# Performance work log

Hardware: AMD Instinct MI355X
Metric: run time of the kernel (lower is better)

The kernel has to match this reference:

```python
import jax, jax.numpy as jnp
import numpy as np
import math
from math import factorial

MUL = 128            # channel multiplicity of in1 and out
LS = [0, 1, 2]       # l values of the three irreps in each input/output
N_PATH_W = MUL * 1 * MUL  # uvw weight block per path (mul2 == 1)

# ---- Wigner 3j (real basis), following e3nn's construction ----

def _su2_cg(j1, m1, j2, m2, j3, m3):
    if m3 != m1 + m2:
        return 0.0
    vmin = int(max(-j1 + j2 + m3, -j1 + m1, 0))
    vmax = int(min(j2 + j3 + m1, j3 - j1 + j2, j3 + m3))
    if vmax < vmin:
        return 0.0
    f = lambda n: factorial(int(round(n)))
    pref = (2 * j3 + 1) * (f(j3 + j1 - j2) * f(j3 - j1 + j2) * f(j1 + j2 - j3) * f(j3 + m3) * f(j3 - m3)) / (
        f(j1 + j2 + j3 + 1) * f(j1 - m1) * f(j1 + m1) * f(j2 - m2) * f(j2 + m2))
    S = 0.0
    for v in range(vmin, vmax + 1):
        S += (-1) ** (v + j2 + m2) * (f(j2 + j3 + m1 - v) * f(j1 - m1 + v)) / (
            f(v) * f(j3 - j1 + j2 - v) * f(j3 + m3 - v) * f(v + j1 - j2 - m3))
    return math.sqrt(pref) * S


def _q(l):
    # change of basis real -> complex spherical harmonics (e3nn convention)
    q = np.zeros((2 * l + 1, 2 * l + 1), dtype=np.complex128)
    for m in range(-l, 0):
        q[l + m, l + abs(m)] = 1 / math.sqrt(2)
        q[l + m, l - abs(m)] = -1j / math.sqrt(2)
    q[l, l] = 1
    for m in range(1, l + 1):
        q[l + m, l + abs(m)] = (-1) ** m / math.sqrt(2)
        q[l + m, l - abs(m)] = 1j * (-1) ** m / math.sqrt(2)
    return (-1j) ** l * q


def _w3j(l1, l2, l3):
    C = np.zeros((2 * l1 + 1, 2 * l2 + 1, 2 * l3 + 1))
    for m1 in range(-l1, l1 + 1):
        for m2 in range(-l2, l2 + 1):
            m3 = m1 + m2
            if abs(m3) <= l3:
                C[m1 + l1, m2 + l2, m3 + l3] = _su2_cg(l1, m1, l2, m2, l3, m3)
    Q1, Q2, Q3 = _q(l1), _q(l2), _q(l3)
    Cc = np.einsum('ij,kl,mn,ikn->jlm', Q1, Q2, np.conj(Q3.T), C.astype(np.complex128))
    Cr, Ci = Cc.real, Cc.imag
    Cp = Cr if np.linalg.norm(Cr) >= np.linalg.norm(Ci) else Ci
    return (Cp / np.linalg.norm(Cp)).astype(np.float32)

# allowed (l1, l2) -> l_out paths for 0e/1o/2e x 0e/1o/2e -> 0e/1o/2e
PATHS = [(0, 0, 0), (0, 1, 1), (0, 2, 2), (1, 0, 1), (1, 1, 0), (1, 1, 2),
         (1, 2, 1), (2, 0, 2), (2, 1, 1), (2, 2, 0), (2, 2, 2)]
# path_normalization='element': alpha = (2*l_out+1) / sum over paths to same out of mul1*mul2
_FAN = {o: sum(MUL for (_, _, c) in PATHS if c == o) for o in LS}
PW = {o: math.sqrt((2 * o + 1) / _FAN[o]) for o in LS}
W3J = {(a, b, c): _w3j(a, b, c) for (a, b, c) in PATHS}


def _split1(x):
    # [N, 1152] -> list of [N, 128, 2l+1]
    parts, off = [], 0
    for l in LS:
        d = MUL * (2 * l + 1)
        parts.append(x[:, off:off + d].reshape(-1, MUL, 2 * l + 1))
        off += d
    return parts


def _split2(x):
    # [N, 9] -> list of [N, 2l+1]
    parts, off = [], 0
    for l in LS:
        parts.append(x[:, off:off + 2 * l + 1])
        off += 2 * l + 1
    return parts


def _fctp(x1, x2, weight):
    xs1, xs2 = _split1(x1), _split2(x2)
    N = x1.shape[0]
    outs = [jnp.zeros((N, MUL, 2 * l + 1), x1.dtype) for l in LS]
    off = 0
    for (l1, l2, lo) in PATHS:
        w = weight[off:off + N_PATH_W].reshape(MUL, MUL)  # [u, w] (v == 1)
        off += N_PATH_W
        C = jnp.asarray(W3J[(l1, l2, lo)])  # [2l1+1, 2l2+1, 2lo+1]
        t = jnp.einsum('ijk,nui,nj->nuk', C, xs1[l1], xs2[l2])
        outs[lo] = outs[lo] + PW[lo] * jnp.einsum('uw,nuk->nwk', w, t)
    return jnp.concatenate([o.reshape(N, -1) for o in outs], axis=1)


def setup_inputs() -> dict:
    key = jax.random.key(0)
    k1, k2, k3 = jax.random.split(key, 3)
    N = 20000
    return {
        'x1': jax.random.normal(k1, (N, MUL * 9), dtype=jnp.float32),
        'x2': jax.random.normal(k2, (N, 9), dtype=jnp.float32),
        'weight': jax.random.normal(k3, (len(PATHS) * N_PATH_W,), dtype=jnp.float32),
    }


def reference(x1, x2, weight):
    return _fctp(x1, x2, weight)
```

## Files before the change

kernel.cpp:

```cpp
#include <hip/hip_runtime.h>
#include <math.h>

#define NPATH 11
#define SROW 1152
#define SAMP 16
#define NTHREADS 512
#define XT_TILE_B 39168

constexpr int H_L1[11]  = {0,0,0,1,1,1,1,2,2,2,2};
constexpr int H_L2[11]  = {0,1,2,0,1,1,2,0,1,2,2};
constexpr int H_LO[11]  = {0,1,2,1,0,2,1,2,1,0,2};
constexpr int H_N1[11]  = {1,1,1,3,3,3,3,5,5,5,5};
constexpr int H_N2[11]  = {1,3,5,1,3,3,5,1,3,5,5};
constexpr int H_N3[11]  = {1,3,5,3,1,5,3,5,3,1,5};
constexpr int H_PIB[12] = {0,1,2,3,6,9,12,15,20,25,30,35};
constexpr int H_MOFF[12]  = {0,1,4,9,18,21,36,45,70,85,90,115};
constexpr int H_W3OFF[12] = {0,1,10,35,44,53,98,143,168,213,238,363};
constexpr int H_X2OFF[3]  = {0,1,4};
constexpr int H_CBASE[3]  = {0,1,4};
constexpr int H_KCB[3]    = {0,1,4};
constexpr float H_PW[3] = {0.05103103630798288f, 0.07654655446197431f, 0.09882117688026186f};

namespace w3c {

constexpr double fact(int n) {
    double r = 1.0;
    for (int i = 2; i <= n; ++i) r *= (double)i;
    return r;
}

constexpr double csqrt(double x) {
    if (x <= 0.0) return 0.0;
    double g = x < 1.0 ? 1.0 : x;
    for (int i = 0; i < 100; ++i) g = 0.5 * (g + x / g);
    return g;
}

constexpr double su2_cg(int j1, int m1, int j2, int m2, int j3, int m3) {
    if (m3 != m1 + m2) return 0.0;
    int vmin = -j1 + j2 + m3;
    if (-j1 + m1 > vmin) vmin = -j1 + m1;
    if (0 > vmin) vmin = 0;
    int vmax = j2 + j3 + m1;
    if (j3 - j1 + j2 < vmax) vmax = j3 - j1 + j2;
    if (j3 + m3 < vmax) vmax = j3 + m3;
    if (vmax < vmin) return 0.0;
    double pref = (2.0 * j3 + 1.0) *
        (fact(j3 + j1 - j2) * fact(j3 - j1 + j2) * fact(j1 + j2 - j3) *
         fact(j3 + m3) * fact(j3 - m3)) /
        (fact(j1 + j2 + j3 + 1) * fact(j1 - m1) * fact(j1 + m1) *
         fact(j2 - m2) * fact(j2 + m2));
    double S = 0.0;
    for (int v = vmin; v <= vmax; ++v) {
        double sgn = ((v + j2 + m2) & 1) ? -1.0 : 1.0;
        S += sgn * (fact(j2 + j3 + m1 - v) * fact(j1 - m1 + v)) /
             (fact(v) * fact(j3 - j1 + j2 - v) * fact(j3 + m3 - v) *
              fact(v + j1 - j2 - m3));
    }
    return csqrt(pref) * S;
}

struct Q { double re[5][5]; double im[5][5]; };

constexpr Q build_q(int l) {
    Q q{};
    double s = csqrt(0.5);
    for (int m = -l; m < 0; ++m) {
        q.re[l + m][l - m] = s;
        q.im[l + m][l + m] = -s;
    }
    q.re[l][l] = 1.0;
    for (int m = 1; m <= l; ++m) {
        double sg = (m & 1) ? -1.0 : 1.0;
        q.re[l + m][l + m] = sg * s;
        q.im[l + m][l - m] = sg * s;
    }
    double fr = 1.0, fi = 0.0;
    if (l == 1) { fr = 0.0; fi = -1.0; }
    else if (l == 2) { fr = -1.0; fi = 0.0; }
    for (int r = 0; r < 5; ++r)
        for (int c = 0; c < 5; ++c) {
            double a = q.re[r][c], b = q.im[r][c];
            q.re[r][c] = a * fr - b * fi;
            q.im[r][c] = a * fi + b * fr;
        }
    return q;
}

struct PathW { float v[125]; };

constexpr PathW make_path(int l1, int l2, int l3) {
    int n1 = 2 * l1 + 1, n2 = 2 * l2 + 1, n3 = 2 * l3 + 1;
    double C[5][5][5] = {};
    for (int m1 = -l1; m1 <= l1; ++m1)
        for (int m2 = -l2; m2 <= l2; ++m2) {
            int m3 = m1 + m2;
            if (m3 >= -l3 && m3 <= l3)
                C[m1 + l1][m2 + l2][m3 + l3] = su2_cg(l1, m1, l2, m2, l3, m3);
        }
    Q q1 = build_q(l1), q2 = build_q(l2), q3 = build_q(l3);

    double Cr[5][5][5] = {}, Ci[5][5][5] = {};
    for (int j = 0; j < n1; ++j)
        for (int l = 0; l < n2; ++l)
            for (int m = 0; m < n3; ++m) {
                double ar = 0.0, ai = 0.0;
                for (int i = 0; i < n1; ++i)
                    for (int k = 0; k < n2; ++k) {
                        double t1r = q1.re[i][j], t1i = q1.im[i][j];
                        double t2r = q2.re[k][l], t2i = q2.im[k][l];
                        double tr = t1r * t2r - t1i * t2i;
                        double ti = t1r * t2i + t1i * t2r;
                        for (int n = 0; n < n3; ++n) {
                            double c = C[i][k][n];
                            if (c == 0.0) continue;
                            double pr = q3.re[n][m], pi = -q3.im[n][m];
                            ar += c * (tr * pr - ti * pi);
                            ai += c * (tr * pi + ti * pr);
                        }
                    }
                Cr[j][l][m] = ar;
                Ci[j][l][m] = ai;
            }

    double nr = 0.0, ni = 0.0;
    for (int j = 0; j < n1; ++j)
        for (int l = 0; l < n2; ++l)
            for (int m = 0; m < n3; ++m) {
                nr += Cr[j][l][m] * Cr[j][l][m];
                ni += Ci[j][l][m] * Ci[j][l][m];
            }
    nr = csqrt(nr);
    ni = csqrt(ni);
    bool useR = (nr >= ni);
    double norm = useR ? nr : ni;

    PathW out{};
    int idx = 0;
    for (int j = 0; j < n1; ++j)
        for (int l = 0; l < n2; ++l)
            for (int m = 0; m < n3; ++m)
                out.v[idx++] = (float)((useR ? Cr[j][l][m] : Ci[j][l][m]) / norm);
    return out;
}

constexpr PathW P0  = make_path(0,0,0);
constexpr PathW P1  = make_path(0,1,1);
constexpr PathW P2  = make_path(0,2,2);
constexpr PathW P3  = make_path(1,0,1);
constexpr PathW P4  = make_path(1,1,0);
constexpr PathW P5  = make_path(1,1,2);
constexpr PathW P6  = make_path(1,2,1);
constexpr PathW P7  = make_path(2,0,2);
constexpr PathW P8  = make_path(2,1,1);
constexpr PathW P9  = make_path(2,2,0);
constexpr PathW P10 = make_path(2,2,2);

struct W3All { float v[363]; };

constexpr W3All make_all() {
    W3All a{};
    const PathW* ps[11] = {&P0,&P1,&P2,&P3,&P4,&P5,&P6,&P7,&P8,&P9,&P10};
    for (int p = 0; p < 11; ++p) {
        int n = H_W3OFF[p+1] - H_W3OFF[p];
        for (int i = 0; i < n; ++i) a.v[H_W3OFF[p] + i] = ps[p]->v[i];
    }
    return a;
}

}

__device__ __constant__ w3c::W3All c_W3 = w3c::make_all();

typedef float f32x4 __attribute__((ext_vector_type(4)));
typedef __bf16 bf16x8 __attribute__((ext_vector_type(8)));

__device__ __forceinline__ unsigned short f2bf(float f) {
    union { float f; unsigned int u; } v; v.f = f;
    unsigned int u = v.u + 0x7fffu + ((v.u >> 16) & 1u);
    return (unsigned short)(u >> 16);
}

#define MFMA(a, b, c) __builtin_amdgcn_mfma_f32_16x16x32_bf16((a), (b), (c), 0, 0, 0)

__device__ __forceinline__ void gll16(const void* g, void* l) {
    __builtin_amdgcn_global_load_lds(
        (const __attribute__((address_space(1))) void*)g,
        (__attribute__((address_space(3))) void*)l,
        16, 0, 0);
}

__global__ __launch_bounds__(256) void wprep_kernel(
    const float* __restrict__ w, unsigned short* __restrict__ whi)
{
    int idx = blockIdx.x * 256 + threadIdx.x;
    if (idx >= NPATH * 128 * 128) return;
    int p   = idx / 16384;
    int rem = idx - p * 16384;
    int wc  = rem >> 7;
    int u   = rem & 127;
    whi[idx] = f2bf(w[p * 16384 + u * 128 + wc]);
}

__global__ __launch_bounds__(256) void xprep_kernel(
    const float* __restrict__ x1, char* __restrict__ xT, long xstride,
    int N)
{
    __shared__ __align__(16) unsigned short sT[9][16][136];
    const int tile = blockIdx.x;
    const int n0   = tile * SAMP;
    const int tid  = threadIdx.x;

    for (int e = tid; e < 9 * 16 * 8; e += 256) {
        int col = e / 128, r = e % 128;
        sT[col][r / 8][128 + (r & 7)] = 0;
    }
    for (int e = tid; e < SAMP * (SROW / 4); e += 256) {
        int n  = e / 288;
        int c4 = (e % 288) * 4;
        f32x4 v = (n0 + n < N) ? *(const f32x4*)&x1[(size_t)(n0 + n) * SROW + c4]
                               : (f32x4)(0.0f);
        #pragma unroll
        for (int j = 0; j < 4; ++j) {
            int c = c4 + j;
            int col, u;
            if (c < 128)       { col = 0;           u = c; }
            else if (c < 512)  { int rr = c - 128;  u = rr / 3; col = 1 + rr % 3; }
            else               { int rr = c - 512;  u = rr / 5; col = 4 + rr % 5; }
            sT[col][n][u] = f2bf(v[j]);
        }
    }
    __syncthreads();
    const char* src = (const char*)&sT[0][0][0];
    char* dst = xT + (size_t)tile * xstride;
    for (int e = tid; e < XT_TILE_B / 16; e += 256)
        *(f32x4*)(dst + e * 16) = *(const f32x4*)(src + e * 16);
}

__device__ __forceinline__ void prefetch_tile(
    const char* __restrict__ gsrc, unsigned char* ldst, int wid, int lane)
{
    #pragma unroll
    for (int c = 0; c < 5; ++c) {
        const int chunk = wid + c * 8;
        if (chunk < 38) {
            gll16(gsrc + chunk * 1024 + lane * 16, ldst + chunk * 1024);
        } else if (chunk == 38) {
            if (lane < 16)
                gll16(gsrc + 38 * 1024 + lane * 16, ldst + 38 * 1024);
        }
    }
}

__device__ __forceinline__ void stage_m35(
    const float* __restrict__ x2, int n0, int N, float* sM35, int tid)
{
    for (int e = tid; e < SAMP * 115; e += NTHREADS) {
        int n = e / 115, m = e % 115;
        float val = 0.0f;
        int pi5 = 0;
        #pragma unroll
        for (int p = 0; p < NPATH; ++p) {
            if (m >= H_MOFF[p] && m < H_MOFF[p + 1]) {
                const int n2 = H_N2[p], n3 = H_N3[p];
                int rr = m - H_MOFF[p];
                int i = rr / n3, k = rr % n3;
                if (n0 + n < N) {
                    const float* Cp  = c_W3.v + H_W3OFF[p];
                    const float* x2p = x2 + (size_t)(n0 + n) * 9 + H_X2OFF[H_L2[p]];
                    float a = 0.0f;
                    #pragma unroll
                    for (int j = 0; j < n2; ++j)
                        a += Cp[(i * n2 + j) * n3 + k] * x2p[j];
                    val = H_PW[H_LO[p]] * a;
                }
                pi5 = (H_PIB[p] + i) * 5 + k;
            }
        }
        sM35[n * 175 + pi5] = val;
    }
}

template<int P0G, int NP, int CB, int NC>
__device__ __forceinline__ void gemm_pass(
    const unsigned short* __restrict__ whi,
    const unsigned short (*sB)[16][136],
    const float* sM35,
    float (&ov)[4][9], int r16, int q4, int wt)
{
    f32x4 acc[NP][NC];
    #pragma unroll
    for (int pp = 0; pp < NP; ++pp)
        #pragma unroll
        for (int i = 0; i < NC; ++i) acc[pp][i] = (f32x4)(0.0f);

    #pragma unroll
    for (int ub = 0; ub < 4; ++ub) {
        const int ko = ub * 32 + q4 * 8;
        bf16x8 B[NC];
        #pragma unroll
        for (int c = 0; c < NC; ++c)
            B[c] = *(const bf16x8*)&sB[CB + c][r16][ko];
        #pragma unroll
        for (int pp = 0; pp < NP; ++pp) {
            const size_t aoff =
                ((size_t)((P0G + pp) * 128 + wt * 16 + r16)) * 128 + ko;
            bf16x8 Ah = *(const bf16x8*)&whi[aoff];
            #pragma unroll
            for (int i = 0; i < NC; ++i)
                acc[pp][i] = MFMA(Ah, B[i], acc[pp][i]);
        }
    }

    #pragma unroll
    for (int pp = 0; pp < NP; ++pp) {
        const int P = P0G + pp;
        #pragma unroll
        for (int i = 0; i < NC; ++i)
            #pragma unroll
            for (int k = 0; k < H_N3[P]; ++k) {
                const float mv = sM35[r16 * 175 + (H_PIB[P] + i) * 5 + k];
                #pragma unroll
                for (int r = 0; r < 4; ++r)
                    ov[r][H_KCB[H_LO[P]] + k] += acc[pp][i][r] * mv;
            }
    }
}

__global__ __launch_bounds__(NTHREADS, 1) void fctp_kernel(
    const float* __restrict__ x2,
    const unsigned short* __restrict__ whi,
    const char* __restrict__ xT, long xstride,
    float* __restrict__ out, int N)
{
    __shared__ __align__(16) unsigned char smem[50368];
    const unsigned short (*sB)[16][136] = (const unsigned short (*)[16][136])smem;
    float* sM35 = (float*)(smem + 39168);

    const int tid  = threadIdx.x;
    const int lane = tid & 63;
    const int wt   = tid >> 6;
    const int r16  = lane & 15;
    const int q4   = lane >> 4;
    const int tile = blockIdx.x;
    const int n0   = tile * SAMP;

    prefetch_tile(xT + (size_t)tile * xstride, smem, wt, lane);
    stage_m35(x2, n0, N, sM35, tid);
    __syncthreads();

    float ov[4][9];
    #pragma unroll
    for (int r = 0; r < 4; ++r)
        #pragma unroll
        for (int j = 0; j < 9; ++j) ov[r][j] = 0.0f;

    gemm_pass<0, 3, 0, 1>(whi, sB, sM35, ov, r16, q4, wt);
    gemm_pass<3, 2, 1, 3>(whi, sB, sM35, ov, r16, q4, wt);
    gemm_pass<5, 2, 1, 3>(whi, sB, sM35, ov, r16, q4, wt);
    gemm_pass<7, 2, 4, 5>(whi, sB, sM35, ov, r16, q4, wt);
    gemm_pass<9, 2, 4, 5>(whi, sB, sM35, ov, r16, q4, wt);

    __syncthreads();
    float* sOut = (float*)smem;
    const int wbase = wt * 16 + q4 * 4;
    #pragma unroll
    for (int half = 0; half < 2; ++half) {
        if ((r16 >> 3) == half) {
            float* so = &sOut[(r16 & 7) * 1156];
            #pragma unroll
            for (int r = 0; r < 4; ++r) {
                const int w = wbase + r;
                so[w] = ov[r][0];
                #pragma unroll
                for (int kk = 0; kk < 3; ++kk) so[128 + w * 3 + kk] = ov[r][1 + kk];
                #pragma unroll
                for (int kk = 0; kk < 5; ++kk) so[512 + w * 5 + kk] = ov[r][4 + kk];
            }
        }
        __syncthreads();
        for (int e = tid; e < 8 * (SROW / 4); e += NTHREADS) {
            int nn = e / (SROW / 4), c4 = (e % (SROW / 4)) * 4;
            int gn = n0 + half * 8 + nn;
            if (gn < N)
                *(f32x4*)&out[(size_t)gn * SROW + c4] =
                    *(const f32x4*)&sOut[nn * 1156 + c4];
        }
        __syncthreads();
    }
}

extern "C" void kernel_launch(void* const* d_in, const int* in_sizes, int n_in,
                              void* d_out, int out_size, void* d_ws, size_t ws_size,
                              hipStream_t stream) {
    const float* x1 = (const float*)d_in[0];
    const float* x2 = (const float*)d_in[1];
    const float* wt = (const float*)d_in[2];
    float* out = (float*)d_out;

    unsigned short* whi = (unsigned short*)d_ws;

    int N = in_sizes[0] / SROW;
    int ntiles = (N + SAMP - 1) / SAMP;

    size_t whiB = (size_t)NPATH * 128 * 128 * sizeof(unsigned short);
    size_t xtB  = (size_t)ntiles * XT_TILE_B;
    char* xT;
    long  xstride;
    if (ws_size >= whiB + xtB) {
        xT = (char*)d_ws + whiB;
        xstride = XT_TILE_B;
    } else {
        xT = (char*)d_out;
        xstride = (long)SAMP * SROW * 4;
    }

    hipLaunchKernelGGL(wprep_kernel, dim3((NPATH * 128 * 128 + 255) / 256),
                       dim3(256), 0, stream, wt, whi);
    hipLaunchKernelGGL(xprep_kernel, dim3(ntiles), dim3(256), 0, stream,
                       x1, xT, xstride, N);

    hipLaunchKernelGGL(fctp_kernel, dim3(ntiles), dim3(NTHREADS), 0, stream,
                       x2, whi, xT, xstride, out, N);
}
```

Measured before the change: 139.3 us.

## Pre-swizzle x1 into MFMA fragment order and read B operands from global

The x1 prep kernel now writes each 16-sample tile in the exact per-lane bf16x8 fragment order the MFMA B operand needs, dropping the padded layout. The main kernel no longer stages the tile into LDS with global_load_lds; each wave loads its B fragments straight from global memory through the cache. The output epilogue is also collapsed from two half-tile passes into one full-tile pass using a larger shared buffer, which removes two barriers. The trade is higher global/L1 load latency inside the MFMA loop, since all 8 waves re-read the same fragments, plus more LDS per block.

```diff
diff --git a/kernel.cpp b/kernel.cpp
--- a/kernel.cpp
+++ b/kernel.cpp
@@ -5,7 +5,7 @@
 #define SROW 1152
 #define SAMP 16
 #define NTHREADS 512
-#define XT_TILE_B 39168
+#define XT2_TILE_B 36864
 
 constexpr int H_L1[11]  = {0,0,0,1,1,1,1,2,2,2,2};
 constexpr int H_L2[11]  = {0,1,2,0,1,1,2,0,1,2,2};
@@ -183,13 +183,6 @@
 
 #define MFMA(a, b, c) __builtin_amdgcn_mfma_f32_16x16x32_bf16((a), (b), (c), 0, 0, 0)
 
-__device__ __forceinline__ void gll16(const void* g, void* l) {
-    __builtin_amdgcn_global_load_lds(
-        (const __attribute__((address_space(1))) void*)g,
-        (__attribute__((address_space(3))) void*)l,
-        16, 0, 0);
-}
-
 __global__ __launch_bounds__(256) void wprep_kernel(
     const float* __restrict__ w, unsigned short* __restrict__ whi)
 {
@@ -206,15 +199,11 @@
     const float* __restrict__ x1, char* __restrict__ xT, long xstride,
     int N)
 {
-    __shared__ __align__(16) unsigned short sT[9][16][136];
+    __shared__ __align__(16) unsigned short sT[9][16][128];
     const int tile = blockIdx.x;
     const int n0   = tile * SAMP;
     const int tid  = threadIdx.x;
 
-    for (int e = tid; e < 9 * 16 * 8; e += 256) {
-        int col = e / 128, r = e % 128;
-        sT[col][r / 8][128 + (r & 7)] = 0;
-    }
     for (int e = tid; e < SAMP * (SROW / 4); e += 256) {
         int n  = e / 288;
         int c4 = (e % 288) * 4;
@@ -231,24 +220,15 @@
         }
     }
     __syncthreads();
-    const char* src = (const char*)&sT[0][0][0];
+
     char* dst = xT + (size_t)tile * xstride;
-    for (int e = tid; e < XT_TILE_B / 16; e += 256)
-        *(f32x4*)(dst + e * 16) = *(const f32x4*)(src + e * 16);
-}
-
-__device__ __forceinline__ void prefetch_tile(
-    const char* __restrict__ gsrc, unsigned char* ldst, int wid, int lane)
-{
-    #pragma unroll
-    for (int c = 0; c < 5; ++c) {
-        const int chunk = wid + c * 8;
-        if (chunk < 38) {
-            gll16(gsrc + chunk * 1024 + lane * 16, ldst + chunk * 1024);
-        } else if (chunk == 38) {
-            if (lane < 16)
-                gll16(gsrc + 38 * 1024 + lane * 16, ldst + 38 * 1024);
-        }
+    for (int e = tid; e < 9 * 4 * 64; e += 256) {
+        int col  = e >> 8;
+        int ub   = (e >> 6) & 3;
+        int lane = e & 63;
+        int r16 = lane & 15, q4 = lane >> 4;
+        const unsigned short* s = &sT[col][r16][ub * 32 + q4 * 8];
+        *(f32x4*)(dst + e * 16) = *(const f32x4*)s;
     }
 }
 
@@ -284,9 +264,9 @@
 template<int P0G, int NP, int CB, int NC>
 __device__ __forceinline__ void gemm_pass(
     const unsigned short* __restrict__ whi,
-    const unsigned short (*sB)[16][136],
+    const char* __restrict__ xt,
     const float* sM35,
-    float (&ov)[4][9], int r16, int q4, int wt)
+    float (&ov)[4][9], int r16, int q4, int wt, int lane)
 {
     f32x4 acc[NP][NC];
     #pragma unroll
@@ -300,7 +280,7 @@
         bf16x8 B[NC];
         #pragma unroll
         for (int c = 0; c < NC; ++c)
-            B[c] = *(const bf16x8*)&sB[CB + c][r16][ko];
+            B[c] = *(const bf16x8*)(xt + (((CB + c) * 4 + ub) << 10) + lane * 16);
         #pragma unroll
         for (int pp = 0; pp < NP; ++pp) {
             const size_t aoff =
@@ -333,9 +313,8 @@
     const char* __restrict__ xT, long xstride,
     float* __restrict__ out, int N)
 {
-    __shared__ __align__(16) unsigned char smem[50368];
-    const unsigned short (*sB)[16][136] = (const unsigned short (*)[16][136])smem;
-    float* sM35 = (float*)(smem + 39168);
+    __shared__ __align__(16) unsigned char smem[73984];
+    float* sM35 = (float*)smem;
 
     const int tid  = threadIdx.x;
     const int lane = tid & 63;
@@ -344,8 +323,8 @@
     const int q4   = lane >> 4;
     const int tile = blockIdx.x;
     const int n0   = tile * SAMP;
-
-    prefetch_tile(xT + (size_t)tile * xstride, smem, wt, lane);
+    const char* xt = xT + (size_t)tile * xstride;
+
     stage_m35(x2, n0, N, sM35, tid);
     __syncthreads();
 
@@ -355,38 +334,35 @@
         #pragma unroll
         for (int j = 0; j < 9; ++j) ov[r][j] = 0.0f;
 
-    gemm_pass<0, 3, 0, 1>(whi, sB, sM35, ov, r16, q4, wt);
-    gemm_pass<3, 2, 1, 3>(whi, sB, sM35, ov, r16, q4, wt);
-    gemm_pass<5, 2, 1, 3>(whi, sB, sM35, ov, r16, q4, wt);
-    gemm_pass<7, 2, 4, 5>(whi, sB, sM35, ov, r16, q4, wt);
-    gemm_pass<9, 2, 4, 5>(whi, sB, sM35, ov, r16, q4, wt);
+    gemm_pass<0, 3, 0, 1>(whi, xt, sM35, ov, r16, q4, wt, lane);
+    gemm_pass<3, 2, 1, 3>(whi, xt, sM35, ov, r16, q4, wt, lane);
+    gemm_pass<5, 2, 1, 3>(whi, xt, sM35, ov, r16, q4, wt, lane);
+    gemm_pass<7, 2, 4, 5>(whi, xt, sM35, ov, r16, q4, wt, lane);
+    gemm_pass<9, 2, 4, 5>(whi, xt, sM35, ov, r16, q4, wt, lane);
 
     __syncthreads();
     float* sOut = (float*)smem;
-    const int wbase = wt * 16 + q4 * 4;
-    #pragma unroll
-    for (int half = 0; half < 2; ++half) {
-        if ((r16 >> 3) == half) {
-            float* so = &sOut[(r16 & 7) * 1156];
+    {
+        const int wbase = wt * 16 + q4 * 4;
+        float* so = &sOut[r16 * 1156];
+        #pragma unroll
+        for (int r = 0; r < 4; ++r) {
+            const int w = wbase + r;
+            so[w] = ov[r][0];
             #pragma unroll
-            for (int r = 0; r < 4; ++r) {
-                const int w = wbase + r;
-                so[w] = ov[r][0];
-                #pragma unroll
-                for (int kk = 0; kk < 3; ++kk) so[128 + w * 3 + kk] = ov[r][1 + kk];
-                #pragma unroll
-                for (int kk = 0; kk < 5; ++kk) so[512 + w * 5 + kk] = ov[r][4 + kk];
-            }
-        }
-        __syncthreads();
-        for (int e = tid; e < 8 * (SROW / 4); e += NTHREADS) {
-            int nn = e / (SROW / 4), c4 = (e % (SROW / 4)) * 4;
-            int gn = n0 + half * 8 + nn;
-            if (gn < N)
-                *(f32x4*)&out[(size_t)gn * SROW + c4] =
-                    *(const f32x4*)&sOut[nn * 1156 + c4];
-        }
-        __syncthreads();
+            for (int kk = 0; kk < 3; ++kk) so[128 + w * 3 + kk] = ov[r][1 + kk];
+            #pragma unroll
+            for (int kk = 0; kk < 5; ++kk) so[512 + w * 5 + kk] = ov[r][4 + kk];
+        }
+    }
+    __syncthreads();
+
+    for (int e = tid; e < SAMP * (SROW / 4); e += NTHREADS) {
+        int nn = e / (SROW / 4), c4 = (e % (SROW / 4)) * 4;
+        int gn = n0 + nn;
+        if (gn < N)
+            *(f32x4*)&out[(size_t)gn * SROW + c4] =
+                *(const f32x4*)&sOut[nn * 1156 + c4];
     }
 }
 
@@ -404,12 +380,12 @@
     int ntiles = (N + SAMP - 1) / SAMP;
 
     size_t whiB = (size_t)NPATH * 128 * 128 * sizeof(unsigned short);
-    size_t xtB  = (size_t)ntiles * XT_TILE_B;
+    size_t xtB  = (size_t)ntiles * XT2_TILE_B;
     char* xT;
     long  xstride;
     if (ws_size >= whiB + xtB) {
         xT = (char*)d_ws + whiB;
-        xstride = XT_TILE_B;
+        xstride = XT2_TILE_B;
     } else {
         xT = (char*)d_out;
         xstride = (long)SAMP * SROW * 4;
```

New measurement: 137.3 us. About the same (-1.5%).
